# Kernel tuning notes

Hardware: AMD Instinct MI355X
Metric: run time of the kernel (lower is better)

Reference implementation:

```python
import jax, jax.numpy as jnp
import numpy as np

N_NODES = 50000
N_EDGES = 800000
IN_FEATS = 256
OUT_FEATS = 128


def setup_inputs() -> dict:
    key = jax.random.key(0)
    k1, k2, k3, k4 = jax.random.split(key, 4)
    feat = jax.random.normal(k1, (N_NODES, IN_FEATS), dtype=jnp.float32)
    # xavier uniform init for weight [in, out]
    limit = float(np.sqrt(6.0 / (IN_FEATS + OUT_FEATS)))
    weight = jax.random.uniform(k2, (IN_FEATS, OUT_FEATS), minval=-limit, maxval=limit, dtype=jnp.float32)
    bias = jnp.zeros((OUT_FEATS,), dtype=jnp.float32)
    src = jax.random.randint(k3, (N_EDGES,), 0, N_NODES, dtype=jnp.int32)
    dst = jax.random.randint(k4, (N_EDGES,), 0, N_NODES, dtype=jnp.int32)
    return {"feat": feat, "weight": weight, "bias": bias, "src": src, "dst": dst}


def reference(feat, weight, bias, src, dst):
    N = feat.shape[0]
    in_f, out_f = weight.shape
    # right normalization: 1 / out_degree(src node), clamped to >= 1
    deg = jax.ops.segment_sum(jnp.ones(src.shape[0], dtype=feat.dtype), src, num_segments=N)
    norm = (1.0 / jnp.maximum(deg, 1.0))[:, None]  # [N,1]
    if in_f > out_f:
        # transform first (cheaper messages), then normalize + aggregate
        h = jnp.matmul(feat, weight) * norm          # [N, out]
        rst = jax.ops.segment_sum(h[src], dst, num_segments=N)  # scatter-sum over edges
    else:
        h = feat * norm                               # [N, in]
        rst = jax.ops.segment_sum(h[src], dst, num_segments=N)
        rst = jnp.matmul(rst, weight)
    return rst + bias
```

## Files before the change

### kernel.cpp

```cpp
#include <hip/hip_runtime.h>

#define N_NODES 50000
#define N_EDGES 800000
#define IN_F 256
#define OUT_F 128

#define CHUNKS 128
#define EPC (N_EDGES / CHUNKS)
#define BINW (N_NODES / 4)
#define NWORDS (N_NODES / 4)
#define RGB 196
#define HIST_BLOCKS (2 * CHUNKS)
#define CPW (CHUNKS / 4)

#define GEMM_BLOCKS 391
#define SCAT_BLOCKS 782

typedef __attribute__((ext_vector_type(8))) short short8;
typedef __attribute__((ext_vector_type(4))) float float4_t;

__device__ __forceinline__ short f2bf(float f) {
  unsigned u = __builtin_bit_cast(unsigned, f);
  u = u + 0x7FFFu + ((u >> 16) & 1u);
  return (short)(u >> 16);
}

__device__ __forceinline__ float bflo(unsigned u) {
  return __builtin_bit_cast(float, u << 16);
}
__device__ __forceinline__ float bfhi(unsigned u) {
  return __builtin_bit_cast(float, u & 0xFFFF0000u);
}

__global__ __launch_bounds__(512) void hist_kernel(const int* __restrict__ src,
                                                   const int* __restrict__ dst,
                                                   unsigned char* __restrict__ pdst8,
                                                   unsigned char* __restrict__ psrc8,
                                                   unsigned char* __restrict__ rank8,
                                                   const float* __restrict__ W,
                                                   short* __restrict__ Wf,
                                                   int* __restrict__ cursor) {
  __shared__ unsigned bins[BINW];
  int b = blockIdx.x;
  int t = threadIdx.x;
  if (b >= HIST_BLOCKS) {
    int bb = b - HIST_BLOCKS;
    if (bb == 0 && t == 0) *cursor = 0;
#pragma unroll
    for (int i = 0; i < 32; ++i) {
      int idx = bb * 16384 + i * 512 + t;
      int k = idx >> 7, n = idx & 127;
      int s = k >> 5, q = (k >> 3) & 3, j = k & 7;
      int tt = n >> 4, m = n & 15;
      Wf[(((s * 8 + tt) * 16 + m) * 32) + q * 8 + j] = f2bf(W[idx]);
    }
    return;
  }
  int h = b >> 7;
  int c = b & 127;
  uint4* b4 = (uint4*)bins;
  for (int j = t; j < BINW / 4; j += 512) b4[j] = (uint4){0u, 0u, 0u, 0u};
  __syncthreads();
  const int* key = h ? src : dst;
  int e0 = c * EPC;

  auto process = [&](int v, int eI) {
    unsigned sh = (v & 3) * 8;
    unsigned old = atomicAdd(&bins[v >> 2], 1u << sh);
    if (!h) rank8[eI] = (unsigned char)((old >> sh) & 0xFFu);
  };

#pragma unroll 2
  for (int tile = 0; tile < 3; ++tile) {
    int i = tile * 2048 + t;
    int k0 = key[e0 + i];
    int k1 = key[e0 + i + 512];
    int k2 = key[e0 + i + 1024];
    int k3 = key[e0 + i + 1536];
    process(k0, e0 + i);
    process(k1, e0 + i + 512);
    process(k2, e0 + i + 1024);
    process(k3, e0 + i + 1536);
  }
  {
    int i = 6144 + t;
    if (i < EPC) process(key[e0 + i], e0 + i);
  }
  __syncthreads();
  uint4* p128 = (uint4*)((h ? psrc8 : pdst8) + (size_t)c * N_NODES);
  const uint4* s128 = (const uint4*)bins;
  for (int j = t; j < BINW / 4; j += 512) p128[j] = s128[j];
}

__global__ __launch_bounds__(256) void reduceoff_kernel(const unsigned char* __restrict__ pdst8,
                                                        const unsigned char* __restrict__ psrc8,
                                                        unsigned char* __restrict__ delta8,
                                                        int* __restrict__ cnt,
                                                        int* __restrict__ row_start,
                                                        int* __restrict__ cursor,
                                                        float* __restrict__ norm) {
  __shared__ unsigned tot[4][64];
  int g = blockIdx.x, side = blockIdx.y;
  int t = threadIdx.x;
  int w = t >> 6, l = t & 63;
  int wd = g * 64 + l;
  bool ok = wd < NWORDS;
  int wdc = ok ? wd : NWORDS - 1;
  const unsigned* P = (const unsigned*)(side == 0 ? pdst8 : psrc8);

  unsigned vals[CPW];
  unsigned s = 0;
#pragma unroll
  for (int i = 0; i < CPW; ++i) {
    vals[i] = P[(size_t)(w * CPW + i) * NWORDS + wdc];
    s += vals[i];
  }
  tot[w][l] = s;
  __syncthreads();

  if (side == 0) {
    unsigned base = 0;
#pragma unroll
    for (int w2 = 0; w2 < 4; ++w2)
      if (w2 < w) base += tot[w2][l];
    unsigned run = base;
    unsigned* D = (unsigned*)delta8;
    if (ok) {
#pragma unroll
      for (int i = 0; i < CPW; ++i) {
        D[(size_t)(w * CPW + i) * NWORDS + wd] = run;
        run += vals[i];
      }
    }
    if (w == 0) {
      unsigned ftot = tot[0][l] + tot[1][l] + tot[2][l] + tot[3][l];
      if (!ok) ftot = 0;
      int c0 = ftot & 255, c1 = (ftot >> 8) & 255, c2 = (ftot >> 16) & 255, c3 = ftot >> 24;
      int T = c0 + c1 + c2 + c3;
      int x = T;
#pragma unroll
      for (int off = 1; off < 64; off <<= 1) {
        int y = __shfl_up(x, off);
        if (l >= off) x += y;
      }
      int waveTotal = __shfl(x, 63);
      int sb = 0;
      if (l == 63) sb = atomicAdd(cursor, waveTotal);
      sb = __shfl(sb, 63);
      int E = sb + x - T;
      if (ok) {
        int4 cv = {c0, c1, c2, c3};
        int4 rv = {E, E + c0, E + c0 + c1, E + c0 + c1 + c2};
        ((int4*)cnt)[wd] = cv;
        ((int4*)row_start)[wd] = rv;
      }
    }
  } else {
    if (w == 0 && ok) {
      unsigned ftot = tot[0][l] + tot[1][l] + tot[2][l] + tot[3][l];
      float4 nv;
      int d0 = ftot & 255, d1 = (ftot >> 8) & 255, d2 = (ftot >> 16) & 255, d3 = (int)(ftot >> 24);
      nv.x = 1.0f / (float)(d0 > 1 ? d0 : 1);
      nv.y = 1.0f / (float)(d1 > 1 ? d1 : 1);
      nv.z = 1.0f / (float)(d2 > 1 ? d2 : 1);
      nv.w = 1.0f / (float)(d3 > 1 ? d3 : 1);
      ((float4*)norm)[wd] = nv;
    }
  }
}

__global__ __launch_bounds__(256) void gemm_kernel(const float* __restrict__ feat,
                                                   const short* __restrict__ Wf,
                                                   const float* __restrict__ norm,
                                                   unsigned short* __restrict__ h) {
  int b = blockIdx.x;
  int tid = threadIdx.x;
  int w = tid >> 6, l = tid & 63;
  int m = l & 15, q = l >> 4;
  long base = (long)b * 128 + w * 32;

  float4_t acc[2][8];
#pragma unroll
  for (int r = 0; r < 2; ++r)
#pragma unroll
    for (int t = 0; t < 8; ++t) acc[r][t] = (float4_t)(0.0f);

  long row0 = base + m;
  long row1 = base + 16 + m;
  long r0c = row0 < N_NODES - 1 ? row0 : N_NODES - 1;
  long r1c = row1 < N_NODES - 1 ? row1 : N_NODES - 1;
  const float* a0p = feat + (size_t)r0c * IN_F;
  const float* a1p = feat + (size_t)r1c * IN_F;
  const short8* bb = (const short8*)Wf;

#pragma unroll
  for (int s = 0; s < 8; ++s) {
    int k0 = s * 32 + q * 8;
    float4_t av0a = *(const float4_t*)(a0p + k0);
    float4_t av0b = *(const float4_t*)(a0p + k0 + 4);
    float4_t av1a = *(const float4_t*)(a1p + k0);
    float4_t av1b = *(const float4_t*)(a1p + k0 + 4);
    short8 fa0, fa1;
#pragma unroll
    for (int i = 0; i < 4; ++i) {
      fa0[i] = f2bf(av0a[i]);
      fa0[i + 4] = f2bf(av0b[i]);
      fa1[i] = f2bf(av1a[i]);
      fa1[i + 4] = f2bf(av1b[i]);
    }
#pragma unroll
    for (int t = 0; t < 8; ++t) {
      short8 fb = bb[((s * 8 + t) * 16 + m) * 4 + q];
      acc[0][t] = __builtin_amdgcn_mfma_f32_16x16x32_bf16(fa0, fb, acc[0][t], 0, 0, 0);
      acc[1][t] = __builtin_amdgcn_mfma_f32_16x16x32_bf16(fa1, fb, acc[1][t], 0, 0, 0);
    }
  }

#pragma unroll
  for (int r = 0; r < 2; ++r) {
#pragma unroll
    for (int i = 0; i < 4; ++i) {
      long row = base + r * 16 + q * 4 + i;
      if (row < N_NODES) {
        float nm = norm[row];
        size_t ho = (size_t)row * OUT_F;
#pragma unroll
        for (int t = 0; t < 8; ++t) {
          h[ho + t * 16 + m] = (unsigned short)f2bf(acc[r][t][i] * nm);
        }
      }
    }
  }
}

__global__ __launch_bounds__(256) void scat_kernel(const int* __restrict__ src,
                                                   const int* __restrict__ dst,
                                                   const int* __restrict__ row_start,
                                                   const unsigned char* __restrict__ delta8,
                                                   const unsigned char* __restrict__ rank8,
                                                   int* __restrict__ eidx) {
  int gt = blockIdx.x * 256 + threadIdx.x;
  int e = gt * 4;
  if (e >= N_EDGES) return;
  int4 d4 = *(const int4*)(dst + e);
  int4 s4 = *(const int4*)(src + e);
  unsigned rr = *(const unsigned*)(rank8 + e);
  int dd[4] = {d4.x, d4.y, d4.z, d4.w};
  int ss[4] = {s4.x, s4.y, s4.z, s4.w};
#pragma unroll
  for (int k = 0; k < 4; ++k) {
    int c = (e + k) / EPC;
    int d = dd[k];
    int pos = row_start[d] + (int)delta8[(size_t)c * N_NODES + d] + (int)((rr >> (8 * k)) & 0xFFu);
    eidx[pos] = ss[k];
  }
}

__global__ __launch_bounds__(256) void agg_kernel(const unsigned short* __restrict__ h,
                                                  const int* __restrict__ row_start,
                                                  const int* __restrict__ cnt,
                                                  const int* __restrict__ eidx,
                                                  const float* __restrict__ bias,
                                                  float* __restrict__ out) {
  int w = threadIdx.x >> 6, l = threadIdx.x & 63;
  int d = blockIdx.x * 4 + w;
  int rs = row_start[d], re = rs + cnt[d];
  const unsigned* __restrict__ hu = (const unsigned*)h;
  int rowsel = l >> 5, cp = l & 31;
  float a0 = 0.f, a1 = 0.f, a2 = 0.f, a3 = 0.f;
  for (int bse = rs; bse < re; bse += 64) {
    int n = re - bse; if (n > 64) n = 64;
    int e = (l < n) ? eidx[bse + l] : 0;
    int half = (n + 1) >> 1;
    int j = 0;
    for (; j + 4 <= half; j += 4) {
      int i0 = 2 * j + rowsel;
      int s0 = __shfl(e, i0);
      int s1 = __shfl(e, i0 + 2);
      int s2 = __shfl(e, i0 + 4);
      int s3 = __shfl(e, i0 + 6);
      uint2 v0 = *(const uint2*)(hu + (size_t)s0 * 64 + 2 * cp);
      uint2 v1 = *(const uint2*)(hu + (size_t)s1 * 64 + 2 * cp);
      uint2 v2 = *(const uint2*)(hu + (size_t)s2 * 64 + 2 * cp);
      uint2 v3 = *(const uint2*)(hu + (size_t)s3 * 64 + 2 * cp);
      if (i0 >= n) { v0.x = 0; v0.y = 0; }
      if (i0 + 2 >= n) { v1.x = 0; v1.y = 0; }
      if (i0 + 4 >= n) { v2.x = 0; v2.y = 0; }
      if (i0 + 6 >= n) { v3.x = 0; v3.y = 0; }
      a0 += bflo(v0.x); a1 += bfhi(v0.x); a2 += bflo(v0.y); a3 += bfhi(v0.y);
      a0 += bflo(v1.x); a1 += bfhi(v1.x); a2 += bflo(v1.y); a3 += bfhi(v1.y);
      a0 += bflo(v2.x); a1 += bfhi(v2.x); a2 += bflo(v2.y); a3 += bfhi(v2.y);
      a0 += bflo(v3.x); a1 += bfhi(v3.x); a2 += bflo(v3.y); a3 += bfhi(v3.y);
    }
    for (; j + 2 <= half; j += 2) {
      int i0 = 2 * j + rowsel;
      int i1 = i0 + 2;
      int s0 = __shfl(e, i0);
      int s1 = __shfl(e, i1);
      uint2 v0 = *(const uint2*)(hu + (size_t)s0 * 64 + 2 * cp);
      uint2 v1 = *(const uint2*)(hu + (size_t)s1 * 64 + 2 * cp);
      if (i0 >= n) { v0.x = 0; v0.y = 0; }
      if (i1 >= n) { v1.x = 0; v1.y = 0; }
      a0 += bflo(v0.x); a1 += bfhi(v0.x); a2 += bflo(v0.y); a3 += bfhi(v0.y);
      a0 += bflo(v1.x); a1 += bfhi(v1.x); a2 += bflo(v1.y); a3 += bfhi(v1.y);
    }
    for (; j < half; ++j) {
      int i0 = 2 * j + rowsel;
      int s0 = __shfl(e, i0);
      uint2 v0 = *(const uint2*)(hu + (size_t)s0 * 64 + 2 * cp);
      if (i0 >= n) { v0.x = 0; v0.y = 0; }
      a0 += bflo(v0.x); a1 += bfhi(v0.x); a2 += bflo(v0.y); a3 += bfhi(v0.y);
    }
  }
  a0 += __shfl_xor(a0, 32);
  a1 += __shfl_xor(a1, 32);
  a2 += __shfl_xor(a2, 32);
  a3 += __shfl_xor(a3, 32);
  if (rowsel == 0) {
    float4 bv = ((const float4*)bias)[cp];
    float4 o;
    o.x = a0 + bv.x; o.y = a1 + bv.y; o.z = a2 + bv.z; o.w = a3 + bv.w;
    ((float4*)(out + (size_t)d * OUT_F))[cp] = o;
  }
}

extern "C" void kernel_launch(void* const* d_in, const int* in_sizes, int n_in,
                              void* d_out, int out_size, void* d_ws, size_t ws_size,
                              hipStream_t stream) {
  const float* feat = (const float*)d_in[0];
  const float* weight = (const float*)d_in[1];
  const float* bias = (const float*)d_in[2];
  const int* src = (const int*)d_in[3];
  const int* dst = (const int*)d_in[4];
  float* out = (float*)d_out;

  char* ws = (char*)d_ws;
  size_t off = 0;
  auto alloc = [&](size_t bytes) -> void* {
    void* p = ws + off;
    off += (bytes + 511) & ~(size_t)511;
    return p;
  };
  int* cursor = (int*)alloc(4);
  int* cnt = (int*)alloc(N_NODES * 4);
  int* row_start = (int*)alloc(N_NODES * 4);
  float* norm = (float*)alloc(N_NODES * 4);
  int* eidx = (int*)alloc(N_EDGES * 4);
  short* Wf = (short*)alloc(IN_F * OUT_F * 2);
  unsigned short* h = (unsigned short*)alloc((size_t)N_NODES * OUT_F * 2);
  unsigned char* pdst8 = (unsigned char*)alloc((size_t)CHUNKS * N_NODES);
  unsigned char* psrc8 = (unsigned char*)alloc((size_t)CHUNKS * N_NODES);
  unsigned char* delta8 = (unsigned char*)alloc((size_t)CHUNKS * N_NODES);
  unsigned char* rank8 = (unsigned char*)alloc((size_t)N_EDGES);
  (void)off; (void)ws_size; (void)in_sizes; (void)n_in; (void)out_size;

  hipLaunchKernelGGL(hist_kernel, dim3(HIST_BLOCKS + 2), dim3(512), 0, stream,
                     src, dst, pdst8, psrc8, rank8, weight, Wf, cursor);
  hipLaunchKernelGGL(reduceoff_kernel, dim3(RGB, 2), dim3(256), 0, stream,
                     pdst8, psrc8, delta8, cnt, row_start, cursor, norm);
  hipLaunchKernelGGL(scat_kernel, dim3(SCAT_BLOCKS), dim3(256), 0, stream,
                     src, dst, row_start, delta8, rank8, eidx);
  hipLaunchKernelGGL(gemm_kernel, dim3(GEMM_BLOCKS), dim3(256), 0, stream,
                     feat, Wf, norm, h);
  hipLaunchKernelGGL(agg_kernel, dim3(N_NODES / 4), dim3(256), 0, stream, h, row_start, cnt, eidx, bias, out);
}
```

Baseline: 184.0 us.

## Fuse GEMM into histogram kernel and apply degree norm during aggregation

The dense feat×W GEMM moves into the first kernel as extra blocks that run alongside the histogram blocks. Each GEMM block converts W to bf16 in shared memory itself rather than reading a pre-swizzled global copy, and the separate gemm launch is removed. Because norm is not known yet when the GEMM runs, the per-source normalization moves into the aggregation kernel as an FMA with norm[src], which adds a scattered norm load per edge. The GEMM blocks now use 512 threads covering 256 rows each and redo the W conversion per block, while the histogram blocks share a 64KB shared allocation.

```diff
diff --git a/kernel.cpp b/kernel.cpp
--- a/kernel.cpp
+++ b/kernel.cpp
@@ -13,7 +13,8 @@
 #define HIST_BLOCKS (2 * CHUNKS)
 #define CPW (CHUNKS / 4)
 
-#define GEMM_BLOCKS 391
+#define GEMM_START HIST_BLOCKS
+#define GEMMF_BLOCKS 196
 #define SCAT_BLOCKS 782
 
 typedef __attribute__((ext_vector_type(8))) short short8;
@@ -32,47 +33,108 @@
   return __builtin_bit_cast(float, u & 0xFFFF0000u);
 }
 
-__global__ __launch_bounds__(512) void hist_kernel(const int* __restrict__ src,
-                                                   const int* __restrict__ dst,
-                                                   unsigned char* __restrict__ pdst8,
-                                                   unsigned char* __restrict__ psrc8,
-                                                   unsigned char* __restrict__ rank8,
-                                                   const float* __restrict__ W,
-                                                   short* __restrict__ Wf,
-                                                   int* __restrict__ cursor) {
-  __shared__ unsigned bins[BINW];
+__global__ __launch_bounds__(512) void fused1_kernel(const int* __restrict__ src,
+                                                     const int* __restrict__ dst,
+                                                     unsigned char* __restrict__ pdst8,
+                                                     unsigned char* __restrict__ psrc8,
+                                                     unsigned char* __restrict__ rank8,
+                                                     const float* __restrict__ W,
+                                                     const float* __restrict__ feat,
+                                                     unsigned short* __restrict__ h,
+                                                     int* __restrict__ cursor) {
+  __shared__ uint4 smem4[4096];
   int b = blockIdx.x;
-  int t = threadIdx.x;
-  if (b >= HIST_BLOCKS) {
-    int bb = b - HIST_BLOCKS;
-    if (bb == 0 && t == 0) *cursor = 0;
-#pragma unroll
-    for (int i = 0; i < 32; ++i) {
-      int idx = bb * 16384 + i * 512 + t;
+  int tid = threadIdx.x;
+
+  if (b >= GEMM_START) {
+    if (b == GEMM_START && tid == 0) *cursor = 0;
+    short* wl = (short*)smem4;
+#pragma unroll
+    for (int i = 0; i < 64; ++i) {
+      int idx = i * 512 + tid;
       int k = idx >> 7, n = idx & 127;
       int s = k >> 5, q = (k >> 3) & 3, j = k & 7;
       int tt = n >> 4, m = n & 15;
-      Wf[(((s * 8 + tt) * 16 + m) * 32) + q * 8 + j] = f2bf(W[idx]);
+      wl[((s * 8 + tt) * 64 + q * 16 + m) * 8 + j] = f2bf(W[idx]);
+    }
+    __syncthreads();
+
+    int w = tid >> 6, l = tid & 63;
+    int m = l & 15, q = l >> 4;
+    long base = (long)(b - GEMM_START) * 256 + w * 32;
+
+    float4_t acc[2][8];
+#pragma unroll
+    for (int r = 0; r < 2; ++r)
+#pragma unroll
+      for (int to = 0; to < 8; ++to) acc[r][to] = (float4_t)(0.0f);
+
+    long row0 = base + m;
+    long row1 = base + 16 + m;
+    long r0c = row0 < N_NODES - 1 ? row0 : N_NODES - 1;
+    long r1c = row1 < N_NODES - 1 ? row1 : N_NODES - 1;
+    const float* a0p = feat + (size_t)r0c * IN_F;
+    const float* a1p = feat + (size_t)r1c * IN_F;
+    const short8* wl8 = (const short8*)smem4;
+
+#pragma unroll
+    for (int s = 0; s < 8; ++s) {
+      int k0 = s * 32 + q * 8;
+      float4_t av0a = *(const float4_t*)(a0p + k0);
+      float4_t av0b = *(const float4_t*)(a0p + k0 + 4);
+      float4_t av1a = *(const float4_t*)(a1p + k0);
+      float4_t av1b = *(const float4_t*)(a1p + k0 + 4);
+      short8 fa0, fa1;
+#pragma unroll
+      for (int i = 0; i < 4; ++i) {
+        fa0[i] = f2bf(av0a[i]);
+        fa0[i + 4] = f2bf(av0b[i]);
+        fa1[i] = f2bf(av1a[i]);
+        fa1[i + 4] = f2bf(av1b[i]);
+      }
+#pragma unroll
+      for (int to = 0; to < 8; ++to) {
+        short8 fb = wl8[(s * 8 + to) * 64 + l];
+        acc[0][to] = __builtin_amdgcn_mfma_f32_16x16x32_bf16(fa0, fb, acc[0][to], 0, 0, 0);
+        acc[1][to] = __builtin_amdgcn_mfma_f32_16x16x32_bf16(fa1, fb, acc[1][to], 0, 0, 0);
+      }
+    }
+
+#pragma unroll
+    for (int r = 0; r < 2; ++r) {
+#pragma unroll
+      for (int i = 0; i < 4; ++i) {
+        long row = base + r * 16 + q * 4 + i;
+        if (row < N_NODES) {
+          size_t ho = (size_t)row * OUT_F;
+#pragma unroll
+          for (int to = 0; to < 8; ++to) {
+            h[ho + to * 16 + m] = (unsigned short)f2bf(acc[r][to][i]);
+          }
+        }
+      }
     }
     return;
   }
-  int h = b >> 7;
+
+  unsigned* bins = (unsigned*)smem4;
+  int hs = b >> 7;
   int c = b & 127;
   uint4* b4 = (uint4*)bins;
-  for (int j = t; j < BINW / 4; j += 512) b4[j] = (uint4){0u, 0u, 0u, 0u};
+  for (int j = tid; j < BINW / 4; j += 512) b4[j] = (uint4){0u, 0u, 0u, 0u};
   __syncthreads();
-  const int* key = h ? src : dst;
+  const int* key = hs ? src : dst;
   int e0 = c * EPC;
 
   auto process = [&](int v, int eI) {
     unsigned sh = (v & 3) * 8;
     unsigned old = atomicAdd(&bins[v >> 2], 1u << sh);
-    if (!h) rank8[eI] = (unsigned char)((old >> sh) & 0xFFu);
+    if (!hs) rank8[eI] = (unsigned char)((old >> sh) & 0xFFu);
   };
 
 #pragma unroll 2
   for (int tile = 0; tile < 3; ++tile) {
-    int i = tile * 2048 + t;
+    int i = tile * 2048 + tid;
     int k0 = key[e0 + i];
     int k1 = key[e0 + i + 512];
     int k2 = key[e0 + i + 1024];
@@ -83,13 +145,13 @@
     process(k3, e0 + i + 1536);
   }
   {
-    int i = 6144 + t;
+    int i = 6144 + tid;
     if (i < EPC) process(key[e0 + i], e0 + i);
   }
   __syncthreads();
-  uint4* p128 = (uint4*)((h ? psrc8 : pdst8) + (size_t)c * N_NODES);
+  uint4* p128 = (uint4*)((hs ? psrc8 : pdst8) + (size_t)c * N_NODES);
   const uint4* s128 = (const uint4*)bins;
-  for (int j = t; j < BINW / 4; j += 512) p128[j] = s128[j];
+  for (int j = tid; j < BINW / 4; j += 512) p128[j] = s128[j];
 }
 
 __global__ __launch_bounds__(256) void reduceoff_kernel(const unsigned char* __restrict__ pdst8,
@@ -169,70 +231,6 @@
   }
 }
 
-__global__ __launch_bounds__(256) void gemm_kernel(const float* __restrict__ feat,
-                                                   const short* __restrict__ Wf,
-                                                   const float* __restrict__ norm,
-                                                   unsigned short* __restrict__ h) {
-  int b = blockIdx.x;
-  int tid = threadIdx.x;
-  int w = tid >> 6, l = tid & 63;
-  int m = l & 15, q = l >> 4;
-  long base = (long)b * 128 + w * 32;
-
-  float4_t acc[2][8];
-#pragma unroll
-  for (int r = 0; r < 2; ++r)
-#pragma unroll
-    for (int t = 0; t < 8; ++t) acc[r][t] = (float4_t)(0.0f);
-
-  long row0 = base + m;
-  long row1 = base + 16 + m;
-  long r0c = row0 < N_NODES - 1 ? row0 : N_NODES - 1;
-  long r1c = row1 < N_NODES - 1 ? row1 : N_NODES - 1;
-  const float* a0p = feat + (size_t)r0c * IN_F;
-  const float* a1p = feat + (size_t)r1c * IN_F;
-  const short8* bb = (const short8*)Wf;
-
-#pragma unroll
-  for (int s = 0; s < 8; ++s) {
-    int k0 = s * 32 + q * 8;
-    float4_t av0a = *(const float4_t*)(a0p + k0);
-    float4_t av0b = *(const float4_t*)(a0p + k0 + 4);
-    float4_t av1a = *(const float4_t*)(a1p + k0);
-    float4_t av1b = *(const float4_t*)(a1p + k0 + 4);
-    short8 fa0, fa1;
-#pragma unroll
-    for (int i = 0; i < 4; ++i) {
-      fa0[i] = f2bf(av0a[i]);
-      fa0[i + 4] = f2bf(av0b[i]);
-      fa1[i] = f2bf(av1a[i]);
-      fa1[i + 4] = f2bf(av1b[i]);
-    }
-#pragma unroll
-    for (int t = 0; t < 8; ++t) {
-      short8 fb = bb[((s * 8 + t) * 16 + m) * 4 + q];
-      acc[0][t] = __builtin_amdgcn_mfma_f32_16x16x32_bf16(fa0, fb, acc[0][t], 0, 0, 0);
-      acc[1][t] = __builtin_amdgcn_mfma_f32_16x16x32_bf16(fa1, fb, acc[1][t], 0, 0, 0);
-    }
-  }
-
-#pragma unroll
-  for (int r = 0; r < 2; ++r) {
-#pragma unroll
-    for (int i = 0; i < 4; ++i) {
-      long row = base + r * 16 + q * 4 + i;
-      if (row < N_NODES) {
-        float nm = norm[row];
-        size_t ho = (size_t)row * OUT_F;
-#pragma unroll
-        for (int t = 0; t < 8; ++t) {
-          h[ho + t * 16 + m] = (unsigned short)f2bf(acc[r][t][i] * nm);
-        }
-      }
-    }
-  }
-}
-
 __global__ __launch_bounds__(256) void scat_kernel(const int* __restrict__ src,
                                                    const int* __restrict__ dst,
                                                    const int* __restrict__ row_start,
@@ -260,6 +258,7 @@
                                                   const int* __restrict__ row_start,
                                                   const int* __restrict__ cnt,
                                                   const int* __restrict__ eidx,
+                                                  const float* __restrict__ norm,
                                                   const float* __restrict__ bias,
                                                   float* __restrict__ out) {
   int w = threadIdx.x >> 6, l = threadIdx.x & 63;
@@ -283,14 +282,19 @@
       uint2 v1 = *(const uint2*)(hu + (size_t)s1 * 64 + 2 * cp);
       uint2 v2 = *(const uint2*)(hu + (size_t)s2 * 64 + 2 * cp);
       uint2 v3 = *(const uint2*)(hu + (size_t)s3 * 64 + 2 * cp);
+      float nm0 = norm[s0], nm1 = norm[s1], nm2 = norm[s2], nm3 = norm[s3];
       if (i0 >= n) { v0.x = 0; v0.y = 0; }
       if (i0 + 2 >= n) { v1.x = 0; v1.y = 0; }
       if (i0 + 4 >= n) { v2.x = 0; v2.y = 0; }
       if (i0 + 6 >= n) { v3.x = 0; v3.y = 0; }
-      a0 += bflo(v0.x); a1 += bfhi(v0.x); a2 += bflo(v0.y); a3 += bfhi(v0.y);
-      a0 += bflo(v1.x); a1 += bfhi(v1.x); a2 += bflo(v1.y); a3 += bfhi(v1.y);
-      a0 += bflo(v2.x); a1 += bfhi(v2.x); a2 += bflo(v2.y); a3 += bfhi(v2.y);
-      a0 += bflo(v3.x); a1 += bfhi(v3.x); a2 += bflo(v3.y); a3 += bfhi(v3.y);
+      a0 = fmaf(bflo(v0.x), nm0, a0); a1 = fmaf(bfhi(v0.x), nm0, a1);
+      a2 = fmaf(bflo(v0.y), nm0, a2); a3 = fmaf(bfhi(v0.y), nm0, a3);
+      a0 = fmaf(bflo(v1.x), nm1, a0); a1 = fmaf(bfhi(v1.x), nm1, a1);
+      a2 = fmaf(bflo(v1.y), nm1, a2); a3 = fmaf(bfhi(v1.y), nm1, a3);
+      a0 = fmaf(bflo(v2.x), nm2, a0); a1 = fmaf(bfhi(v2.x), nm2, a1);
+      a2 = fmaf(bflo(v2.y), nm2, a2); a3 = fmaf(bfhi(v2.y), nm2, a3);
+      a0 = fmaf(bflo(v3.x), nm3, a0); a1 = fmaf(bfhi(v3.x), nm3, a1);
+      a2 = fmaf(bflo(v3.y), nm3, a2); a3 = fmaf(bfhi(v3.y), nm3, a3);
     }
     for (; j + 2 <= half; j += 2) {
       int i0 = 2 * j + rowsel;
@@ -299,17 +303,22 @@
       int s1 = __shfl(e, i1);
       uint2 v0 = *(const uint2*)(hu + (size_t)s0 * 64 + 2 * cp);
       uint2 v1 = *(const uint2*)(hu + (size_t)s1 * 64 + 2 * cp);
+      float nm0 = norm[s0], nm1 = norm[s1];
       if (i0 >= n) { v0.x = 0; v0.y = 0; }
       if (i1 >= n) { v1.x = 0; v1.y = 0; }
-      a0 += bflo(v0.x); a1 += bfhi(v0.x); a2 += bflo(v0.y); a3 += bfhi(v0.y);
-      a0 += bflo(v1.x); a1 += bfhi(v1.x); a2 += bflo(v1.y); a3 += bfhi(v1.y);
+      a0 = fmaf(bflo(v0.x), nm0, a0); a1 = fmaf(bfhi(v0.x), nm0, a1);
+      a2 = fmaf(bflo(v0.y), nm0, a2); a3 = fmaf(bfhi(v0.y), nm0, a3);
+      a0 = fmaf(bflo(v1.x), nm1, a0); a1 = fmaf(bfhi(v1.x), nm1, a1);
+      a2 = fmaf(bflo(v1.y), nm1, a2); a3 = fmaf(bfhi(v1.y), nm1, a3);
     }
     for (; j < half; ++j) {
       int i0 = 2 * j + rowsel;
       int s0 = __shfl(e, i0);
       uint2 v0 = *(const uint2*)(hu + (size_t)s0 * 64 + 2 * cp);
+      float nm0 = norm[s0];
       if (i0 >= n) { v0.x = 0; v0.y = 0; }
-      a0 += bflo(v0.x); a1 += bfhi(v0.x); a2 += bflo(v0.y); a3 += bfhi(v0.y);
+      a0 = fmaf(bflo(v0.x), nm0, a0); a1 = fmaf(bfhi(v0.x), nm0, a1);
+      a2 = fmaf(bflo(v0.y), nm0, a2); a3 = fmaf(bfhi(v0.y), nm0, a3);
     }
   }
   a0 += __shfl_xor(a0, 32);
@@ -346,7 +355,6 @@
   int* row_start = (int*)alloc(N_NODES * 4);
   float* norm = (float*)alloc(N_NODES * 4);
   int* eidx = (int*)alloc(N_EDGES * 4);
-  short* Wf = (short*)alloc(IN_F * OUT_F * 2);
   unsigned short* h = (unsigned short*)alloc((size_t)N_NODES * OUT_F * 2);
   unsigned char* pdst8 = (unsigned char*)alloc((size_t)CHUNKS * N_NODES);
   unsigned char* psrc8 = (unsigned char*)alloc((size_t)CHUNKS * N_NODES);
@@ -354,13 +362,12 @@
   unsigned char* rank8 = (unsigned char*)alloc((size_t)N_EDGES);
   (void)off; (void)ws_size; (void)in_sizes; (void)n_in; (void)out_size;
 
-  hipLaunchKernelGGL(hist_kernel, dim3(HIST_BLOCKS + 2), dim3(512), 0, stream,
-                     src, dst, pdst8, psrc8, rank8, weight, Wf, cursor);
+  hipLaunchKernelGGL(fused1_kernel, dim3(HIST_BLOCKS + GEMMF_BLOCKS), dim3(512), 0, stream,
+                     src, dst, pdst8, psrc8, rank8, weight, feat, h, cursor);
   hipLaunchKernelGGL(reduceoff_kernel, dim3(RGB, 2), dim3(256), 0, stream,
                      pdst8, psrc8, delta8, cnt, row_start, cursor, norm);
   hipLaunchKernelGGL(scat_kernel, dim3(SCAT_BLOCKS), dim3(256), 0, stream,
                      src, dst, row_start, delta8, rank8, eidx);
-  hipLaunchKernelGGL(gemm_kernel, dim3(GEMM_BLOCKS), dim3(256), 0, stream,
-                     feat, Wf, norm, h);
-  hipLaunchKernelGGL(agg_kernel, dim3(N_NODES / 4), dim3(256), 0, stream, h, row_start, cnt, eidx, bias, out);
-}
+  hipLaunchKernelGGL(agg_kernel, dim3(N_NODES / 4), dim3(256), 0, stream,
+                     h, row_start, cnt, eidx, norm, bias, out);
+}
```

After: 170.7 us. 7.2% less time.
